# Kernel optimization log

Hardware: AMD Instinct MI355X
Metric: run time of the kernel (lower is better)

## Reference

```python
import jax, jax.numpy as jnp
import numpy as np

D, H, W, VP = 10, 400, 352, 35  # grid depth/height/width, points per voxel
C1_IN, C1_H = 7, 16   # VFE-1: Linear 7->16, concat -> 32
C2_IN, C2_H = 32, 64  # VFE-2: Linear 32->64, concat -> 128
BN_EPS = 1e-5


def setup_inputs() -> dict:
    key = jax.random.key(0)
    ks = jax.random.split(key, 12)
    K = 15000
    feature = jax.random.normal(ks[0], (K, VP, C1_IN), jnp.float32)
    keep = (jax.random.uniform(ks[1], (K, VP, 1)) < 0.8).astype(jnp.float32)
    feature = feature * keep
    bs = 1
    coordinate = jnp.concatenate([
        jax.random.randint(ks[2], (K, 1), 0, bs),
        jax.random.randint(ks[3], (K, 1), 0, D),
        jax.random.randint(ks[4], (K, 1), 0, H),
        jax.random.randint(ks[5], (K, 1), 0, W),
    ], axis=1).astype(jnp.int32)
    w1 = jax.random.normal(ks[6], (C1_IN, C1_H), jnp.float32) * 0.3
    b1 = jnp.zeros((C1_H,), jnp.float32)
    g1 = jnp.ones((C1_H,), jnp.float32)
    be1 = jnp.zeros((C1_H,), jnp.float32)
    w2 = jax.random.normal(ks[7], (C2_IN, C2_H), jnp.float32) * 0.15
    b2 = jnp.zeros((C2_H,), jnp.float32)
    g2 = jnp.ones((C2_H,), jnp.float32)
    be2 = jnp.zeros((C2_H,), jnp.float32)
    return dict(feature=feature, coordinate=coordinate, bs=bs,
                w1=w1, b1=b1, g1=g1, be1=be1,
                w2=w2, b2=b2, g2=g2, be2=be2)


def _vfe(x, mask, Wm, b, gamma, beta):
    # Linear + ReLU, then BatchNorm1d (training-mode batch stats over (K, VP))
    pw = jax.nn.relu(jnp.einsum('kpi,ih->kph', x, Wm) + b)
    mean = jnp.mean(pw, axis=(0, 1))
    var = jnp.var(pw, axis=(0, 1))  # biased variance, as BN uses for normalization
    pw = (pw - mean) * jax.lax.rsqrt(var + BN_EPS) * gamma + beta
    agg = jnp.max(pw, axis=1, keepdims=True)            # [K,1,Ch] per-voxel max
    concat = jnp.concatenate([pw, jnp.broadcast_to(agg, pw.shape)], axis=-1)
    return concat * mask                                  # mask broadcasts [K,VP,1]


def reference(feature, coordinate, bs, w1, b1, g1, be1, w2, b2, g2, be2):
    # mask: point is valid if max over its 7 features != 0
    mask = (jnp.max(feature, axis=2, keepdims=True) != 0).astype(feature.dtype)
    x = _vfe(feature, mask, w1, b1, g1, be1)   # [K,VP,32]
    x = _vfe(x, mask, w2, b2, g2, be2)         # [K,VP,128]
    voxelwise = jnp.max(x, axis=1)             # [K,128]
    c = coordinate
    out = jnp.zeros((bs, D, H, W, 2 * C2_H), feature.dtype)
    # sparse -> dense sums duplicate coordinates, matching torch.sparse to_dense
    out = out.at[c[:, 0], c[:, 1], c[:, 2], c[:, 3]].add(voxelwise)
    return out
```

## Files before the change

### kernel.cpp

```cpp
#include <hip/hip_runtime.h>
#include <math.h>

#define VPTS 35
#define CIN1 7
#define CH1  16
#define CH2  64
#define DD   10
#define HHH  400
#define WWW  352
#define BN_EPS 1e-5f


__global__ void k_init(float* __restrict__ ws) {
  if (threadIdx.x < 320) ws[threadIdx.x] = 0.f;
}

__global__ void __launch_bounds__(256) k_A(
    const float* __restrict__ feat,
    const float* __restrict__ w1, const float* __restrict__ b1,
    float* __restrict__ red1, float4* __restrict__ out4, long zA, int KP) {
  float w[CIN1][CH1], bb[CH1];
#pragma unroll
  for (int i = 0; i < CIN1; ++i)
#pragma unroll
    for (int c = 0; c < CH1; ++c) w[i][c] = w1[i * CH1 + c];
#pragma unroll
  for (int c = 0; c < CH1; ++c) bb[c] = b1[c];
  float s[CH1], q[CH1];
#pragma unroll
  for (int c = 0; c < CH1; ++c) { s[c] = 0.f; q[c] = 0.f; }
  int tid = blockIdx.x * blockDim.x + threadIdx.x;
  int stride = gridDim.x * blockDim.x;
  for (int idx = tid; idx < KP; idx += stride) {
    float x[CIN1];
#pragma unroll
    for (int i = 0; i < CIN1; ++i) x[i] = feat[(size_t)idx * CIN1 + i];
#pragma unroll
    for (int c = 0; c < CH1; ++c) {
      float a = bb[c];
#pragma unroll
      for (int i = 0; i < CIN1; ++i) a = fmaf(x[i], w[i][c], a);
      a = fmaxf(a, 0.f);
      s[c] += a;
      q[c] = fmaf(a, a, q[c]);
    }
  }
  float4 z = make_float4(0.f, 0.f, 0.f, 0.f);
  for (long i = tid; i < zA; i += stride) out4[i] = z;
  __shared__ float ssum[2 * CH1];
  if (threadIdx.x < 2 * CH1) ssum[threadIdx.x] = 0.f;
  __syncthreads();
#pragma unroll
  for (int c = 0; c < CH1; ++c) {
    float a = s[c], b = q[c];
    for (int o = 32; o > 0; o >>= 1) {
      a += __shfl_down(a, o);
      b += __shfl_down(b, o);
    }
    if ((threadIdx.x & 63) == 0) {
      atomicAdd(&ssum[c], a);
      atomicAdd(&ssum[CH1 + c], b);
    }
  }
  __syncthreads();
  if (threadIdx.x < 2 * CH1) atomicAdd(&red1[threadIdx.x], ssum[threadIdx.x]);
}

__global__ void __launch_bounds__(256) k_heavy(
    const float* __restrict__ feat,
    const float* __restrict__ w1, const float* __restrict__ b1,
    const float* __restrict__ g1, const float* __restrict__ be1,
    const float* __restrict__ red1,
    const float* __restrict__ w2, const float* __restrict__ b2,
    const float* __restrict__ g2,
    float* __restrict__ red2,
    float* __restrict__ E1buf, float* __restrict__ E2buf,
    float* __restrict__ FLbuf, int K,
    float4* __restrict__ out4, long z0, long n4, float invN) {
  __shared__ __align__(16) float fs_s[4][248];
  __shared__ __align__(16) float pw1_s[4][560];
  __shared__ __align__(16) float agg1_s[4][16];
  __shared__ float ss[2 * CH2];
  int t = threadIdx.x, lane = t & 63, w = t >> 6;
  float* fs   = fs_s[w];
  float* pw1  = pw1_s[w];
  float* agg1 = agg1_s[w];

  int c1 = lane & 15;
  float mean1 = red1[c1] * invN;
  float var1  = red1[CH1 + c1] * invN - mean1 * mean1;
  float sc1   = g1[c1] * rsqrtf(var1 + BN_EPS);
  float sh1   = be1[c1] - mean1 * sc1;
  float b1c   = b1[c1];
  float w1r[CIN1];
#pragma unroll
  for (int j = 0; j < CIN1; ++j) w1r[j] = w1[j * CH1 + c1];
  float wcol[32];
#pragma unroll
  for (int i = 0; i < 32; ++i) wcol[i] = w2[i * CH2 + lane];
  float b2c = b2[lane];
  float sgn = (g2[lane] >= 0.f) ? 1.f : -1.f;

  float lsum = 0.f, lsq = 0.f;
  int waveg = blockIdx.x * 4 + w;
  int nwave = gridDim.x * 4;
  for (int k = waveg; k < K; k += nwave) {
    for (int i = lane; i < VPTS * CIN1; i += 64) fs[i] = feat[(size_t)k * (VPTS * CIN1) + i];
    bool vbit = false;
    if (lane < VPTS) {
      float m = fs[lane * CIN1];
#pragma unroll
      for (int j = 1; j < CIN1; ++j) m = fmaxf(m, fs[lane * CIN1 + j]);
      vbit = (m != 0.f);
    }
    unsigned long long mbits = __ballot(vbit);
#pragma unroll
    for (int j = 0; j < 9; ++j) {
      int idx = lane + 64 * j;
      if (idx < VPTS * CH1) {
        int p = idx >> 4;
        float a = b1c;
#pragma unroll
        for (int jj = 0; jj < CIN1; ++jj) a = fmaf(fs[p * CIN1 + jj], w1r[jj], a);
        a = fmaxf(a, 0.f);
        pw1[idx] = fmaf(a, sc1, sh1);
      }
    }
    {
      int g = lane >> 4;
      float am = -INFINITY;
      for (int p = g; p < VPTS; p += 4) am = fmaxf(am, pw1[p * CH1 + c1]);
      am = fmaxf(am, __shfl_xor(am, 16));
      am = fmaxf(am, __shfl_xor(am, 32));
      if (lane < CH1) agg1[lane] = am;
    }
    float aggdot = 0.f;
    {
      const float4* a4 = (const float4*)agg1;
#pragma unroll
      for (int i = 0; i < 4; ++i) {
        float4 v = a4[i];
        aggdot = fmaf(v.x, wcol[16 + 4 * i + 0], aggdot);
        aggdot = fmaf(v.y, wcol[16 + 4 * i + 1], aggdot);
        aggdot = fmaf(v.z, wcol[16 + 4 * i + 2], aggdot);
        aggdot = fmaf(v.w, wcol[16 + 4 * i + 3], aggdot);
      }
    }
    float E1w = -INFINITY, E2w = -INFINITY;
    const float4* p4 = (const float4*)pw1;
    for (int p = 0; p < VPTS; ++p) {
      float4 v0 = p4[p * 4 + 0], v1 = p4[p * 4 + 1];
      float4 v2 = p4[p * 4 + 2], v3 = p4[p * 4 + 3];
      float low = 0.f;
      low = fmaf(v0.x, wcol[0], low);  low = fmaf(v0.y, wcol[1], low);
      low = fmaf(v0.z, wcol[2], low);  low = fmaf(v0.w, wcol[3], low);
      low = fmaf(v1.x, wcol[4], low);  low = fmaf(v1.y, wcol[5], low);
      low = fmaf(v1.z, wcol[6], low);  low = fmaf(v1.w, wcol[7], low);
      low = fmaf(v2.x, wcol[8], low);  low = fmaf(v2.y, wcol[9], low);
      low = fmaf(v2.z, wcol[10], low); low = fmaf(v2.w, wcol[11], low);
      low = fmaf(v3.x, wcol[12], low); low = fmaf(v3.y, wcol[13], low);
      low = fmaf(v3.z, wcol[14], low); low = fmaf(v3.w, wcol[15], low);
      bool valid = (mbits >> p) & 1ull;
      float m = valid ? 1.f : 0.f;
      float pw2 = fmaxf(fmaf(m, low + aggdot, b2c), 0.f);
      lsum += pw2;
      lsq = fmaf(pw2, pw2, lsq);
      float sp = sgn * pw2;
      E2w = fmaxf(E2w, sp);
      if (valid) E1w = fmaxf(E1w, sp);
    }
    E1buf[(size_t)k * 64 + lane] = E1w;
    E2buf[(size_t)k * 64 + lane] = E2w;
    if (lane == 0) FLbuf[k] = (float)__popcll(mbits);
  }
  {
    float4 zv = make_float4(0.f, 0.f, 0.f, 0.f);
    long stride = (long)gridDim.x * 256;
    for (long zi = z0 + (long)blockIdx.x * 256 + t; zi < n4; zi += stride)
      out4[zi] = zv;
  }
  if (t < 2 * CH2) ss[t] = 0.f;
  __syncthreads();
  atomicAdd(&ss[lane], lsum);
  atomicAdd(&ss[CH2 + lane], lsq);
  __syncthreads();
  if (t < 2 * CH2) atomicAdd(&red2[t], ss[t]);
}

__global__ void __launch_bounds__(256) k_scatter(
    const float* __restrict__ E1buf, const float* __restrict__ E2buf,
    const float* __restrict__ FLbuf, const float* __restrict__ red2,
    const float* __restrict__ g2, const float* __restrict__ be2,
    const int* __restrict__ coord, float* __restrict__ out, int K,
    float invN) {
  __shared__ float scsh2_s[2 * CH2];
  int t = threadIdx.x;
  if (t < CH2) {
    float mean = red2[t] * invN;
    float var = red2[CH2 + t] * invN - mean * mean;
    float inv = rsqrtf(var + BN_EPS);
    float sc = g2[t] * inv;
    scsh2_s[t] = sc;
    scsh2_s[CH2 + t] = be2[t] - mean * sc;
  }
  __syncthreads();
  int k = blockIdx.x * 2 + (t >> 7);
  if (k >= K) return;
  int tl = t & 127;
  int c = tl & 63;
  float nv = FLbuf[k];
  bool anyV = nv > 0.f;
  bool anyI = nv < (float)VPTS;
  float sc = scsh2_s[c], sh = scsh2_s[CH2 + c];
  float cand = -INFINITY;
  if (anyV) {
    float E = (tl < 64) ? E1buf[(size_t)k * 64 + c] : E2buf[(size_t)k * 64 + c];
    cand = fmaf(fabsf(sc), E, sh);
  }
  if (anyI) cand = fmaxf(cand, 0.f);
  int4 cc = *reinterpret_cast<const int4*>(coord + (size_t)k * 4);
  long vox = ((long)(cc.x * DD + cc.y) * HHH + cc.z) * WWW + cc.w;
  atomicAdd(&out[vox * (2 * CH2) + tl], cand);
}

__global__ void __launch_bounds__(256) k_zero(float4* __restrict__ out4,
                                              long n4, float* __restrict__ ws) {
  long i = (long)blockIdx.x * blockDim.x + threadIdx.x;
  long stride = (long)gridDim.x * blockDim.x;
  float4 z = make_float4(0.f, 0.f, 0.f, 0.f);
  for (; i < n4; i += stride) out4[i] = z;
  if (blockIdx.x == 0 && threadIdx.x < 320) ws[threadIdx.x] = 0.f;
}

__global__ void k_finalize(const float* __restrict__ red,
                           const float* __restrict__ g,
                           const float* __restrict__ be,
                           float* __restrict__ scsh, int CH, float invN) {
  int c = threadIdx.x;
  if (c < CH) {
    float mean = red[c] * invN;
    float var = red[CH + c] * invN - mean * mean;
    float inv = rsqrtf(var + BN_EPS);
    float sc = g[c] * inv;
    scsh[c] = sc;
    scsh[CH + c] = be[c] - mean * sc;
  }
}

__global__ void __launch_bounds__(256) k_stats1_fb(
    const float* __restrict__ feat,
    const float* __restrict__ w1, const float* __restrict__ b1,
    float* __restrict__ red1, int KP) {
  float w[CIN1][CH1], bb[CH1];
#pragma unroll
  for (int i = 0; i < CIN1; ++i)
#pragma unroll
    for (int c = 0; c < CH1; ++c) w[i][c] = w1[i * CH1 + c];
#pragma unroll
  for (int c = 0; c < CH1; ++c) bb[c] = b1[c];
  float s[CH1], q[CH1];
#pragma unroll
  for (int c = 0; c < CH1; ++c) { s[c] = 0.f; q[c] = 0.f; }
  int tid = blockIdx.x * blockDim.x + threadIdx.x;
  int stride = gridDim.x * blockDim.x;
  for (int idx = tid; idx < KP; idx += stride) {
    float x[CIN1];
#pragma unroll
    for (int i = 0; i < CIN1; ++i) x[i] = feat[(size_t)idx * CIN1 + i];
#pragma unroll
    for (int c = 0; c < CH1; ++c) {
      float a = bb[c];
#pragma unroll
      for (int i = 0; i < CIN1; ++i) a = fmaf(x[i], w[i][c], a);
      a = fmaxf(a, 0.f);
      s[c] += a;
      q[c] = fmaf(a, a, q[c]);
    }
  }
  __shared__ float ssum[2 * CH1];
  if (threadIdx.x < 2 * CH1) ssum[threadIdx.x] = 0.f;
  __syncthreads();
#pragma unroll
  for (int c = 0; c < CH1; ++c) {
    float a = s[c], b = q[c];
    for (int o = 32; o > 0; o >>= 1) {
      a += __shfl_down(a, o);
      b += __shfl_down(b, o);
    }
    if ((threadIdx.x & 63) == 0) {
      atomicAdd(&ssum[c], a);
      atomicAdd(&ssum[CH1 + c], b);
    }
  }
  __syncthreads();
  if (threadIdx.x < 2 * CH1) atomicAdd(&red1[threadIdx.x], ssum[threadIdx.x]);
}

__device__ __forceinline__ void compute_x2_old(
    const float* __restrict__ feat, int k, int t,
    const float* __restrict__ w1, const float* __restrict__ b1,
    const float* __restrict__ scsh1,
    float* fs, float* mask_s, float* pw1_s, float* agg1_s, float* x2_s) {
  if (t < VPTS * CIN1) fs[t] = feat[(size_t)k * (VPTS * CIN1) + t];
  __syncthreads();
  if (t < VPTS) {
    float m = fs[t * CIN1];
#pragma unroll
    for (int i = 1; i < CIN1; ++i) m = fmaxf(m, fs[t * CIN1 + i]);
    mask_s[t] = (m != 0.f) ? 1.f : 0.f;
  }
  for (int i = t; i < VPTS * CH1; i += 256) {
    int p = i >> 4, c = i & 15;
    float acc = b1[c];
#pragma unroll
    for (int j = 0; j < CIN1; ++j) acc = fmaf(fs[p * CIN1 + j], w1[j * CH1 + c], acc);
    acc = fmaxf(acc, 0.f);
    pw1_s[i] = fmaf(acc, scsh1[c], scsh1[CH1 + c]);
  }
  __syncthreads();
  if (t < CH1) {
    float m = pw1_s[t];
    for (int p = 1; p < VPTS; ++p) m = fmaxf(m, pw1_s[p * CH1 + t]);
    agg1_s[t] = m;
  }
  __syncthreads();
  for (int i = t; i < VPTS * 32; i += 256) {
    int p = i >> 5, c = i & 31;
    x2_s[i] = (c < CH1 ? pw1_s[p * CH1 + c] : agg1_s[c - CH1]) * mask_s[p];
  }
  __syncthreads();
}

__global__ void __launch_bounds__(256) k_stats2_old(
    const float* __restrict__ feat,
    const float* __restrict__ w1, const float* __restrict__ b1,
    const float* __restrict__ scsh1,
    const float* __restrict__ w2, const float* __restrict__ b2,
    float* __restrict__ red2, int K) {
  __shared__ float fs[VPTS * CIN1], mask_s[VPTS], pw1_s[VPTS * CH1], agg1_s[CH1];
  __shared__ __align__(16) float x2_s[VPTS * 32];
  __shared__ __align__(16) float w2_s[32 * CH2];
  __shared__ float ss[2 * CH2];
  int t = threadIdx.x;
  for (int i = t; i < 32 * CH2; i += 256) w2_s[i] = w2[i];
  if (t < 2 * CH2) ss[t] = 0.f;
  __syncthreads();
  int c = t & 63;
  float wcol[32];
#pragma unroll
  for (int i = 0; i < 32; ++i) wcol[i] = w2_s[i * CH2 + c];
  float bb = b2[c];
  float lsum = 0.f, lsq = 0.f;
  for (int k = blockIdx.x; k < K; k += gridDim.x) {
    compute_x2_old(feat, k, t, w1, b1, scsh1, fs, mask_s, pw1_s, agg1_s, x2_s);
    for (int p = t >> 6; p < VPTS; p += 4) {
      const float4* xv = (const float4*)(x2_s + p * 32);
      float a = bb;
#pragma unroll
      for (int i = 0; i < 8; ++i) {
        float4 v = xv[i];
        a = fmaf(v.x, wcol[4 * i + 0], a);
        a = fmaf(v.y, wcol[4 * i + 1], a);
        a = fmaf(v.z, wcol[4 * i + 2], a);
        a = fmaf(v.w, wcol[4 * i + 3], a);
      }
      a = fmaxf(a, 0.f);
      lsum += a;
      lsq = fmaf(a, a, lsq);
    }
  }
  atomicAdd(&ss[c], lsum);
  atomicAdd(&ss[CH2 + c], lsq);
  __syncthreads();
  if (t < 2 * CH2) atomicAdd(&red2[t], ss[t]);
}

__global__ void __launch_bounds__(256) k_final_old(
    const float* __restrict__ feat,
    const float* __restrict__ w1, const float* __restrict__ b1,
    const float* __restrict__ scsh1,
    const float* __restrict__ w2, const float* __restrict__ b2,
    const float* __restrict__ scsh2,
    const int* __restrict__ coord,
    float* __restrict__ out, int K) {
  __shared__ float fs[VPTS * CIN1], mask_s[VPTS], pw1_s[VPTS * CH1], agg1_s[CH1];
  __shared__ __align__(16) float x2_s[VPTS * 32];
  __shared__ __align__(16) float w2_s[32 * CH2];
  __shared__ float pw2_s[VPTS * CH2];
  __shared__ float agg2_s[CH2];
  int t = threadIdx.x;
  for (int i = t; i < 32 * CH2; i += 256) w2_s[i] = w2[i];
  __syncthreads();
  int c = t & 63;
  float wcol[32];
#pragma unroll
  for (int i = 0; i < 32; ++i) wcol[i] = w2_s[i * CH2 + c];
  float bb = b2[c];
  float sc = scsh2[c], sh = scsh2[CH2 + c];
  for (int k = blockIdx.x; k < K; k += gridDim.x) {
    compute_x2_old(feat, k, t, w1, b1, scsh1, fs, mask_s, pw1_s, agg1_s, x2_s);
    for (int p = t >> 6; p < VPTS; p += 4) {
      const float4* xv = (const float4*)(x2_s + p * 32);
      float a = bb;
#pragma unroll
      for (int i = 0; i < 8; ++i) {
        float4 v = xv[i];
        a = fmaf(v.x, wcol[4 * i + 0], a);
        a = fmaf(v.y, wcol[4 * i + 1], a);
        a = fmaf(v.z, wcol[4 * i + 2], a);
        a = fmaf(v.w, wcol[4 * i + 3], a);
      }
      a = fmaxf(a, 0.f);
      pw2_s[p * CH2 + c] = fmaf(a, sc, sh);
    }
    __syncthreads();
    if (t < CH2) {
      float m = pw2_s[t];
      for (int p = 1; p < VPTS; ++p) m = fmaxf(m, pw2_s[p * CH2 + t]);
      agg2_s[t] = m;
    }
    __syncthreads();
    if (t < 2 * CH2) {
      float vm = -INFINITY;
      if (t < CH2) {
        for (int p = 0; p < VPTS; ++p) vm = fmaxf(vm, pw2_s[p * CH2 + t] * mask_s[p]);
      } else {
        float a = agg2_s[t - CH2];
        for (int p = 0; p < VPTS; ++p) vm = fmaxf(vm, a * mask_s[p]);
      }
      int4 cc = *reinterpret_cast<const int4*>(coord + (size_t)k * 4);
      long vox = ((long)(cc.x * DD + cc.y) * HHH + cc.z) * WWW + cc.w;
      atomicAdd(&out[vox * (2 * CH2) + t], vm);
    }
  }
}

extern "C" void kernel_launch(void* const* d_in, const int* in_sizes, int n_in,
                              void* d_out, int out_size, void* d_ws, size_t ws_size,
                              hipStream_t stream) {
  const float* feat = (const float*)d_in[0];
  const int* coord  = (const int*)d_in[1];
  const float* w1  = (const float*)d_in[3];
  const float* b1  = (const float*)d_in[4];
  const float* g1  = (const float*)d_in[5];
  const float* be1 = (const float*)d_in[6];
  const float* w2  = (const float*)d_in[7];
  const float* b2  = (const float*)d_in[8];
  const float* g2  = (const float*)d_in[9];
  const float* be2 = (const float*)d_in[10];
  float* out = (float*)d_out;
  float* ws = (float*)d_ws;

  int K = in_sizes[0] / (VPTS * CIN1);
  int KP = K * VPTS;
  float invN = 1.f / (float)KP;

  float* red1  = ws;
  float* scsh1 = ws + 32;
  float* red2  = ws + 64;
  float* scsh2 = ws + 192;
  float* E1buf = ws + 1024;
  float* E2buf = E1buf + (size_t)64 * K;
  float* FLbuf = E2buf + (size_t)64 * K;

  size_t need_bytes = (1024 + (size_t)K * 129) * sizeof(float);

  long n4 = (long)out_size / 4;
  long zA = (n4 * 55) / 100;

  if (ws_size >= need_bytes) {
    k_init<<<1, 320, 0, stream>>>(ws);
    k_A<<<2048, 256, 0, stream>>>(feat, w1, b1, red1, (float4*)out, zA, KP);
    k_heavy<<<2048, 256, 0, stream>>>(feat, w1, b1, g1, be1, red1,
                                      w2, b2, g2, red2, E1buf, E2buf, FLbuf, K,
                                      (float4*)out, zA, n4, invN);
    k_scatter<<<(K + 1) / 2, 256, 0, stream>>>(E1buf, E2buf, FLbuf, red2,
                                               g2, be2, coord, out, K, invN);
  } else {
    k_zero<<<2048, 256, 0, stream>>>((float4*)out, n4, ws);
    k_stats1_fb<<<512, 256, 0, stream>>>(feat, w1, b1, red1, KP);
    k_finalize<<<1, 64, 0, stream>>>(red1, g1, be1, scsh1, CH1, invN);
    k_stats2_old<<<1024, 256, 0, stream>>>(feat, w1, b1, scsh1, w2, b2, red2, K);
    k_finalize<<<1, 64, 0, stream>>>(red2, g2, be2, scsh2, CH2, invN);
    k_final_old<<<2048, 256, 0, stream>>>(feat, w1, b1, scsh1, w2, b2, scsh2,
                                          coord, out, K);
  }
}
```

Before: 202.2 us.

## Stripe BN stat atomics and interleave output zeroing into heavy voxel loop

Splits the global BatchNorm sum/sumsq accumulators into 8 stripes selected by block index, so the 2048 blocks' final atomics contend on separate addresses; consumers sum the stripes when computing mean and variance. The tail zero-fill of the dense output in k_heavy is also moved inside the per-voxel loop (20 float4 stores per iteration), so memory stores overlap with compute instead of running as a separate phase at the end. This costs a larger workspace layout, an 8-way read when finalizing stats, and extra store traffic mixed into the compute loop.

```diff
diff --git a/kernel.cpp b/kernel.cpp
--- a/kernel.cpp
+++ b/kernel.cpp
@@ -9,16 +9,17 @@
 #define HHH  400
 #define WWW  352
 #define BN_EPS 1e-5f
+#define NSTRIPE 8
 
 
 __global__ void k_init(float* __restrict__ ws) {
-  if (threadIdx.x < 320) ws[threadIdx.x] = 0.f;
+  for (int i = threadIdx.x; i < 1280; i += blockDim.x) ws[i] = 0.f;
 }
 
 __global__ void __launch_bounds__(256) k_A(
     const float* __restrict__ feat,
     const float* __restrict__ w1, const float* __restrict__ b1,
-    float* __restrict__ red1, float4* __restrict__ out4, long zA, int KP) {
+    float* __restrict__ red1p, float4* __restrict__ out4, long zA, int KP) {
   float w[CIN1][CH1], bb[CH1];
 #pragma unroll
   for (int i = 0; i < CIN1; ++i)
@@ -63,17 +64,19 @@
     }
   }
   __syncthreads();
-  if (threadIdx.x < 2 * CH1) atomicAdd(&red1[threadIdx.x], ssum[threadIdx.x]);
+  if (threadIdx.x < 2 * CH1)
+    atomicAdd(&red1p[(blockIdx.x & (NSTRIPE - 1)) * 2 * CH1 + threadIdx.x],
+              ssum[threadIdx.x]);
 }
 
 __global__ void __launch_bounds__(256) k_heavy(
     const float* __restrict__ feat,
     const float* __restrict__ w1, const float* __restrict__ b1,
     const float* __restrict__ g1, const float* __restrict__ be1,
-    const float* __restrict__ red1,
+    const float* __restrict__ red1p,
     const float* __restrict__ w2, const float* __restrict__ b2,
     const float* __restrict__ g2,
-    float* __restrict__ red2,
+    float* __restrict__ red2p,
     float* __restrict__ E1buf, float* __restrict__ E2buf,
     float* __restrict__ FLbuf, int K,
     float4* __restrict__ out4, long z0, long n4, float invN) {
@@ -87,8 +90,14 @@
   float* agg1 = agg1_s[w];
 
   int c1 = lane & 15;
-  float mean1 = red1[c1] * invN;
-  float var1  = red1[CH1 + c1] * invN - mean1 * mean1;
+  float r1s = 0.f, r1q = 0.f;
+#pragma unroll
+  for (int sIdx = 0; sIdx < NSTRIPE; ++sIdx) {
+    r1s += red1p[sIdx * 2 * CH1 + c1];
+    r1q += red1p[sIdx * 2 * CH1 + CH1 + c1];
+  }
+  float mean1 = r1s * invN;
+  float var1  = r1q * invN - mean1 * mean1;
   float sc1   = g1[c1] * rsqrtf(var1 + BN_EPS);
   float sh1   = be1[c1] - mean1 * sc1;
   float b1c   = b1[c1];
@@ -104,8 +113,12 @@
   float lsum = 0.f, lsq = 0.f;
   int waveg = blockIdx.x * 4 + w;
   int nwave = gridDim.x * 4;
+  long zstride = (long)gridDim.x * 256;
+  long zi = z0 + (long)blockIdx.x * 256 + t;
+  float4 zv = make_float4(0.f, 0.f, 0.f, 0.f);
   for (int k = waveg; k < K; k += nwave) {
-    for (int i = lane; i < VPTS * CIN1; i += 64) fs[i] = feat[(size_t)k * (VPTS * CIN1) + i];
+    for (int i = lane; i < VPTS * CIN1; i += 64)
+      fs[i] = feat[(size_t)k * (VPTS * CIN1) + i];
     bool vbit = false;
     if (lane < VPTS) {
       float m = fs[lane * CIN1];
@@ -133,6 +146,10 @@
       am = fmaxf(am, __shfl_xor(am, 16));
       am = fmaxf(am, __shfl_xor(am, 32));
       if (lane < CH1) agg1[lane] = am;
+    }
+#pragma unroll
+    for (int u = 0; u < 20; ++u) {
+      if (zi < n4) { out4[zi] = zv; zi += zstride; }
     }
     float aggdot = 0.f;
     {
@@ -173,31 +190,33 @@
     E2buf[(size_t)k * 64 + lane] = E2w;
     if (lane == 0) FLbuf[k] = (float)__popcll(mbits);
   }
-  {
-    float4 zv = make_float4(0.f, 0.f, 0.f, 0.f);
-    long stride = (long)gridDim.x * 256;
-    for (long zi = z0 + (long)blockIdx.x * 256 + t; zi < n4; zi += stride)
-      out4[zi] = zv;
-  }
+  for (; zi < n4; zi += zstride) out4[zi] = zv;
   if (t < 2 * CH2) ss[t] = 0.f;
   __syncthreads();
   atomicAdd(&ss[lane], lsum);
   atomicAdd(&ss[CH2 + lane], lsq);
   __syncthreads();
-  if (t < 2 * CH2) atomicAdd(&red2[t], ss[t]);
+  if (t < 2 * CH2)
+    atomicAdd(&red2p[(blockIdx.x & (NSTRIPE - 1)) * 2 * CH2 + t], ss[t]);
 }
 
 __global__ void __launch_bounds__(256) k_scatter(
     const float* __restrict__ E1buf, const float* __restrict__ E2buf,
-    const float* __restrict__ FLbuf, const float* __restrict__ red2,
+    const float* __restrict__ FLbuf, const float* __restrict__ red2p,
     const float* __restrict__ g2, const float* __restrict__ be2,
     const int* __restrict__ coord, float* __restrict__ out, int K,
     float invN) {
   __shared__ float scsh2_s[2 * CH2];
   int t = threadIdx.x;
   if (t < CH2) {
-    float mean = red2[t] * invN;
-    float var = red2[CH2 + t] * invN - mean * mean;
+    float rs = 0.f, rq = 0.f;
+#pragma unroll
+    for (int sIdx = 0; sIdx < NSTRIPE; ++sIdx) {
+      rs += red2p[sIdx * 2 * CH2 + t];
+      rq += red2p[sIdx * 2 * CH2 + CH2 + t];
+    }
+    float mean = rs * invN;
+    float var = rq * invN - mean * mean;
     float inv = rsqrtf(var + BN_EPS);
     float sc = g2[t] * inv;
     scsh2_s[t] = sc;
@@ -224,12 +243,12 @@
 }
 
 __global__ void __launch_bounds__(256) k_zero(float4* __restrict__ out4,
-                                              long n4, float* __restrict__ ws) {
+                                              long n4, float* __restrict__ wsfb) {
   long i = (long)blockIdx.x * blockDim.x + threadIdx.x;
   long stride = (long)gridDim.x * blockDim.x;
   float4 z = make_float4(0.f, 0.f, 0.f, 0.f);
   for (; i < n4; i += stride) out4[i] = z;
-  if (blockIdx.x == 0 && threadIdx.x < 320) ws[threadIdx.x] = 0.f;
+  if (blockIdx.x == 0 && threadIdx.x < 320) wsfb[threadIdx.x] = 0.f;
 }
 
 __global__ void k_finalize(const float* __restrict__ red,
@@ -455,29 +474,32 @@
   int KP = K * VPTS;
   float invN = 1.f / (float)KP;
 
-  float* red1  = ws;
-  float* scsh1 = ws + 32;
-  float* red2  = ws + 64;
-  float* scsh2 = ws + 192;
-  float* E1buf = ws + 1024;
+  float* red1p = ws;
+  float* red2p = ws + 256;
+  float* fb    = ws + 1280;
+  float* E1buf = ws + 2048;
   float* E2buf = E1buf + (size_t)64 * K;
   float* FLbuf = E2buf + (size_t)64 * K;
 
-  size_t need_bytes = (1024 + (size_t)K * 129) * sizeof(float);
+  size_t need_bytes = (2048 + (size_t)K * 129) * sizeof(float);
 
   long n4 = (long)out_size / 4;
   long zA = (n4 * 55) / 100;
 
   if (ws_size >= need_bytes) {
-    k_init<<<1, 320, 0, stream>>>(ws);
-    k_A<<<2048, 256, 0, stream>>>(feat, w1, b1, red1, (float4*)out, zA, KP);
-    k_heavy<<<2048, 256, 0, stream>>>(feat, w1, b1, g1, be1, red1,
-                                      w2, b2, g2, red2, E1buf, E2buf, FLbuf, K,
+    k_init<<<1, 1024, 0, stream>>>(ws);
+    k_A<<<2048, 256, 0, stream>>>(feat, w1, b1, red1p, (float4*)out, zA, KP);
+    k_heavy<<<2048, 256, 0, stream>>>(feat, w1, b1, g1, be1, red1p,
+                                      w2, b2, g2, red2p, E1buf, E2buf, FLbuf, K,
                                       (float4*)out, zA, n4, invN);
-    k_scatter<<<(K + 1) / 2, 256, 0, stream>>>(E1buf, E2buf, FLbuf, red2,
+    k_scatter<<<(K + 1) / 2, 256, 0, stream>>>(E1buf, E2buf, FLbuf, red2p,
                                                g2, be2, coord, out, K, invN);
   } else {
-    k_zero<<<2048, 256, 0, stream>>>((float4*)out, n4, ws);
+    float* red1  = fb;
+    float* scsh1 = fb + 32;
+    float* red2  = fb + 64;
+    float* scsh2 = fb + 192;
+    k_zero<<<2048, 256, 0, stream>>>((float4*)out, n4, fb);
     k_stats1_fb<<<512, 256, 0, stream>>>(feat, w1, b1, red1, KP);
     k_finalize<<<1, 64, 0, stream>>>(red1, g1, be1, scsh1, CH1, invN);
     k_stats2_old<<<1024, 256, 0, stream>>>(feat, w1, b1, scsh1, w2, b2, red2, K);
```

New measurement: 194.4 us. 1.04x faster.
